# Kernel optimization log

Hardware: AMD Instinct MI355X
Metric: run time of the kernel (lower is better)

## Reference

```python
import jax, jax.numpy as jnp
import numpy as np

N_HEADS = 16

def _rotate_half(x):
    half = x.shape[-1] // 2
    x1, x2 = x[..., :half], x[..., half:]
    return jnp.concatenate([-x2, x1], axis=-1)

def setup_inputs() -> dict:
    key = jax.random.key(0)
    ks = jax.random.split(key, 6)
    B, L, D = 8, 1024, 1280
    hd = D // N_HEADS
    return {
        "hidden_states": jax.random.normal(ks[0], (B, L, D), dtype=jnp.float32),
        "rotary_pos_emb": jax.random.normal(ks[1], (L, hd // 2), dtype=jnp.float32),
        "W_qkv": jax.random.normal(ks[2], (D, 3 * D), dtype=jnp.float32) * 0.02,
        "b_qkv": jax.random.normal(ks[3], (3 * D,), dtype=jnp.float32) * 0.02,
        "W_proj": jax.random.normal(ks[4], (D, D), dtype=jnp.float32) * 0.02,
        "b_proj": jax.random.normal(ks[5], (D,), dtype=jnp.float32) * 0.02,
    }

def reference(hidden_states, rotary_pos_emb, W_qkv, b_qkv, W_proj, b_proj):
    B, L, D = hidden_states.shape
    H = N_HEADS
    hd = D // H
    # QKV projection -> [3, B, H, L, hd]
    qkv = (hidden_states @ W_qkv + b_qkv).reshape(B, L, 3, H, hd)
    qkv = jnp.transpose(qkv, (2, 0, 3, 1, 4))
    q, k, v = qkv[0], qkv[1], qkv[2]
    # rotary embedding: emb = cat([freqs, freqs]) -> [L, hd], broadcast [1,1,L,hd]
    emb = jnp.concatenate([rotary_pos_emb, rotary_pos_emb], axis=-1)
    cos = jnp.cos(emb)[None, None]
    sin = jnp.sin(emb)[None, None]
    q = q * cos + _rotate_half(q) * sin
    k = k * cos + _rotate_half(k) * sin
    # causal SDPA (cu_seqlens is None => is_causal=True)
    scale = 1.0 / jnp.sqrt(jnp.asarray(hd, dtype=q.dtype))
    scores = jnp.einsum("bhqd,bhkd->bhqk", q, k) * scale
    causal = jnp.tril(jnp.ones((L, L), dtype=bool))
    scores = jnp.where(causal, scores, jnp.finfo(scores.dtype).min)
    attn = jax.nn.softmax(scores, axis=-1)
    out = jnp.einsum("bhqk,bhkd->bhqd", attn, v)  # [B,H,L,hd]
    out = jnp.transpose(out, (0, 2, 1, 3)).reshape(B, L, D)
    return out @ W_proj + b_proj
```

## Files before the change

### kernel.cpp

```cpp
#include <hip/hip_runtime.h>
#include <hip/hip_bf16.h>
#include <stdint.h>

#define DEV static __device__ __forceinline__

typedef __attribute__((ext_vector_type(4))) float  f32x4;
typedef __attribute__((ext_vector_type(8))) __bf16 bf16x8;
typedef __attribute__((ext_vector_type(8))) unsigned short u16x8;
typedef __attribute__((ext_vector_type(4))) unsigned short u16x4;
typedef __attribute__((ext_vector_type(4))) float  fvec4;

#define SC2F 0.16129870963914802f

DEV unsigned short f2b(float f) {
  __bf16 h = (__bf16)f;
  unsigned short u; __builtin_memcpy(&u, &h, 2);
  return u;
}
DEV float b2f(unsigned short b) {
  union { unsigned int u; float f; } v; v.u = ((unsigned int)b) << 16;
  return v.f;
}
DEV bf16x8 bzero8() {
  u16x8 z = 0; bf16x8 r; __builtin_memcpy(&r, &z, 16); return r;
}

DEV void gload_lds16(const void* g, void* l) {
  __builtin_amdgcn_global_load_lds(
      (__attribute__((address_space(1))) void*)(uintptr_t)g,
      (__attribute__((address_space(3))) void*)(uintptr_t)l, 16, 0, 0);
}


__global__ void convert_bf16x4(const float* __restrict__ in,
                               unsigned short* __restrict__ out, int n4) {
  int i = blockIdx.x * 256 + threadIdx.x;
  if (i >= n4) return;
  fvec4 v = *(const fvec4*)&in[(size_t)i * 4];
  u16x4 o;
  o[0] = f2b(v[0]); o[1] = f2b(v[1]); o[2] = f2b(v[2]); o[3] = f2b(v[3]);
  *(u16x4*)&out[(size_t)i * 4] = o;
}

__global__ void transpose_f2b(const float* __restrict__ in,
                              unsigned short* __restrict__ out, int R, int C) {
  __shared__ float t[32][33];
  int c0 = blockIdx.x * 32, r0 = blockIdx.y * 32;
  int tx = threadIdx.x & 31, ty = threadIdx.x >> 5;
#pragma unroll
  for (int i = 0; i < 32; i += 8)
    t[ty + i][tx] = in[(size_t)(r0 + ty + i) * C + c0 + tx];
  __syncthreads();
#pragma unroll
  for (int i = 0; i < 32; i += 8)
    out[(size_t)(c0 + ty + i) * R + r0 + tx] = f2b(t[tx][ty + i]);
}

__global__ void rope_table(const float* __restrict__ r, float* __restrict__ c,
                           float* __restrict__ s, int n) {
  int i = blockIdx.x * 256 + threadIdx.x;
  if (i < n) { float v = r[i]; c[i] = cosf(v); s[i] = sinf(v); }
}

template <int EPI>
__global__ __launch_bounds__(512, 2) void gemm256(
    const unsigned short* __restrict__ A, const unsigned short* __restrict__ Bt,
    const float* __restrict__ bias,
    unsigned short* __restrict__ qo, unsigned short* __restrict__ ko,
    unsigned short* __restrict__ vo, float* __restrict__ outf,
    int M, int N, int K) {
  __shared__ __align__(16) unsigned short As[2][256 * 64];
  __shared__ __align__(16) unsigned short Bs[2][256 * 64];
  const int tid = threadIdx.x;
  const int lane = tid & 63, wave = tid >> 6;
  const int wr = wave >> 2, wc = wave & 3;
  const int g = lane >> 4, lr = lane & 15;
  const int nwg = gridDim.x, cpx = nwg >> 3;
  const int swz = (blockIdx.x & 7) * cpx + (blockIdx.x >> 3);
  const int gx = N >> 8;
  const int bx = swz % gx, by = swz / gx;
  const int m0 = by * 256, n0 = bx * 256;
  const int nt = K >> 6;

  f32x4 acc[8][4];
#pragma unroll
  for (int i = 0; i < 8; ++i)
#pragma unroll
    for (int j = 0; j < 4; ++j) acc[i][j] = f32x4{0.f, 0.f, 0.f, 0.f};

#define STAGE256(bi, t)                                                       \
  {                                                                           \
    const int k0s = (t) * 64;                                                 \
    _Pragma("unroll")                                                         \
    for (int it = 0; it < 4; ++it) {                                          \
      int e = (it * 512 + tid) * 8;                                           \
      int r = e >> 6, p = (e >> 3) & 7;                                       \
      int sc = ((p ^ (r & 7)) << 3);                                          \
      gload_lds16(&A[(size_t)(m0 + r) * K + k0s + sc], &As[bi][e]);           \
      gload_lds16(&Bt[(size_t)(n0 + r) * K + k0s + sc], &Bs[bi][e]);          \
    }                                                                         \
  }

  STAGE256(0, 0);
  __syncthreads();

  for (int t = 0; t < nt; ++t) {
    const int cur = t & 1;
    if (t + 1 < nt) STAGE256(cur ^ 1, t + 1);
#pragma unroll
    for (int kk = 0; kk < 2; ++kk) {
      bf16x8 av[8], bv[4];
#pragma unroll
      for (int mf = 0; mf < 8; ++mf) {
        int row = wr * 128 + mf * 16 + lr;
        int ch = (kk * 4 + g) ^ (row & 7);
        av[mf] = *(const bf16x8*)&As[cur][row * 64 + ch * 8];
      }
#pragma unroll
      for (int nf = 0; nf < 4; ++nf) {
        int row = wc * 64 + nf * 16 + lr;
        int ch = (kk * 4 + g) ^ (row & 7);
        bv[nf] = *(const bf16x8*)&Bs[cur][row * 64 + ch * 8];
      }
#pragma unroll
      for (int mf = 0; mf < 8; ++mf)
#pragma unroll
        for (int nf = 0; nf < 4; ++nf)
          acc[mf][nf] = __builtin_amdgcn_mfma_f32_16x16x32_bf16(
              av[mf], bv[nf], acc[mf][nf], 0, 0, 0);
    }
    __syncthreads();
  }
#undef STAGE256

  if (EPI == 0) {
#pragma unroll
    for (int nf = 0; nf < 4; ++nf) {
      int col = n0 + wc * 64 + nf * 16 + lr;
      float bvv = bias[col];
      int s = col / 1280;
      int rem = col - s * 1280;
      int h = rem / 80, d = rem - h * 80;
      unsigned short* dst = (s == 0) ? qo : ((s == 1) ? ko : vo);
#pragma unroll
      for (int mf = 0; mf < 8; ++mf) {
#pragma unroll
        for (int r = 0; r < 4; ++r) {
          int row = m0 + wr * 128 + mf * 16 + g * 4 + r;
          int b = row >> 10, l = row & 1023;
          dst[((size_t)(b * 16 + h) * 1024 + l) * 80 + d] =
              f2b(acc[mf][nf][r] + bvv);
        }
      }
    }
  } else {
#pragma unroll
    for (int mf = 0; mf < 8; ++mf) {
#pragma unroll
      for (int r = 0; r < 4; ++r) {
        int row = m0 + wr * 128 + mf * 16 + g * 4 + r;
#pragma unroll
        for (int nf = 0; nf < 4; ++nf) {
          int col = n0 + wc * 64 + nf * 16 + lr;
          outf[(size_t)row * N + col] = acc[mf][nf][r] + bias[col];
        }
      }
    }
  }
}

template <int EPI>
__global__ __launch_bounds__(256) void gemm128(
    const unsigned short* __restrict__ A, const unsigned short* __restrict__ Bt,
    const float* __restrict__ bias,
    unsigned short* __restrict__ qo, unsigned short* __restrict__ ko,
    unsigned short* __restrict__ vo, float* __restrict__ outf,
    int M, int N, int K) {
  __shared__ __align__(16) unsigned short As[128 * 64];
  __shared__ __align__(16) unsigned short Bs[128 * 64];
  const int tid = threadIdx.x;
  const int lane = tid & 63, wave = tid >> 6;
  const int wr = wave >> 1, wc = wave & 1;
  const int g = lane >> 4, lr = lane & 15;
  const int nwg = gridDim.x, cpx = nwg >> 3;
  const int swz = (blockIdx.x & 7) * cpx + (blockIdx.x >> 3);
  const int gx = N >> 7;
  const int bx = swz % gx, by = swz / gx;
  const int m0 = by * 128, n0 = bx * 128;

  f32x4 acc[4][4];
#pragma unroll
  for (int i = 0; i < 4; ++i)
#pragma unroll
    for (int j = 0; j < 4; ++j) acc[i][j] = f32x4{0.f, 0.f, 0.f, 0.f};

  for (int k0 = 0; k0 < K; k0 += 64) {
#pragma unroll
    for (int it = 0; it < 4; ++it) {
      int e = (it * 256 + tid) * 8;
      int r = e >> 6, p = (e >> 3) & 7;
      int sc = ((p ^ (r & 7)) << 3);
      gload_lds16(&A[(size_t)(m0 + r) * K + k0 + sc], &As[e]);
      gload_lds16(&Bt[(size_t)(n0 + r) * K + k0 + sc], &Bs[e]);
    }
    __syncthreads();
#pragma unroll
    for (int kk = 0; kk < 2; ++kk) {
      bf16x8 av[4], bv[4];
#pragma unroll
      for (int mf = 0; mf < 4; ++mf) {
        int row = wr * 64 + mf * 16 + lr;
        int ch = (kk * 4 + g) ^ (row & 7);
        av[mf] = *(const bf16x8*)&As[row * 64 + ch * 8];
      }
#pragma unroll
      for (int nf = 0; nf < 4; ++nf) {
        int row = wc * 64 + nf * 16 + lr;
        int ch = (kk * 4 + g) ^ (row & 7);
        bv[nf] = *(const bf16x8*)&Bs[row * 64 + ch * 8];
      }
#pragma unroll
      for (int mf = 0; mf < 4; ++mf)
#pragma unroll
        for (int nf = 0; nf < 4; ++nf)
          acc[mf][nf] = __builtin_amdgcn_mfma_f32_16x16x32_bf16(
              av[mf], bv[nf], acc[mf][nf], 0, 0, 0);
    }
    __syncthreads();
  }

  if (EPI == 0) {
#pragma unroll
    for (int nf = 0; nf < 4; ++nf) {
      int col = n0 + wc * 64 + nf * 16 + lr;
      float bvv = bias[col];
      int s = col / 1280;
      int rem = col - s * 1280;
      int h = rem / 80, d = rem - h * 80;
      unsigned short* dst = (s == 0) ? qo : ((s == 1) ? ko : vo);
#pragma unroll
      for (int mf = 0; mf < 4; ++mf) {
#pragma unroll
        for (int r = 0; r < 4; ++r) {
          int row = m0 + wr * 64 + mf * 16 + g * 4 + r;
          int b = row >> 10, l = row & 1023;
          dst[((size_t)(b * 16 + h) * 1024 + l) * 80 + d] =
              f2b(acc[mf][nf][r] + bvv);
        }
      }
    }
  } else {
#pragma unroll
    for (int mf = 0; mf < 4; ++mf) {
#pragma unroll
      for (int r = 0; r < 4; ++r) {
        int row = m0 + wr * 64 + mf * 16 + g * 4 + r;
#pragma unroll
        for (int nf = 0; nf < 4; ++nf) {
          int col = n0 + wc * 64 + nf * 16 + lr;
          outf[(size_t)row * N + col] = acc[mf][nf][r] + bias[col];
        }
      }
    }
  }
}

__global__ void rope_apply(unsigned short* __restrict__ q0,
                           unsigned short* __restrict__ q1,
                           const float* __restrict__ cosT,
                           const float* __restrict__ sinT) {
  int i = blockIdx.x * 256 + threadIdx.x;
  if (i >= 2 * 131072 * 5) return;
  bool isq = (i < 131072 * 5);
  unsigned short* arr = isq ? q0 : q1;
  float sc = isq ? SC2F : 1.0f;
  int rem = isq ? i : (i - 131072 * 5);
  int row = rem / 5, c = rem - (rem / 5) * 5;
  int l = row & 1023;
  size_t base = (size_t)row * 80 + c * 8;
  u16x8 x1 = *(const u16x8*)&arr[base];
  u16x8 x2 = *(const u16x8*)&arr[base + 40];
  const float* cp = &cosT[l * 40 + c * 8];
  const float* sp = &sinT[l * 40 + c * 8];
  u16x8 y1, y2;
#pragma unroll
  for (int j = 0; j < 8; ++j) {
    float a = b2f(x1[j]), b = b2f(x2[j]);
    float cc = cp[j], ss = sp[j];
    y1[j] = f2b((a * cc - b * ss) * sc);
    y2[j] = f2b((b * cc + a * ss) * sc);
  }
  *(u16x8*)&arr[base] = y1;
  *(u16x8*)&arr[base + 40] = y2;
}

__global__ __launch_bounds__(512, 4) void attn_fwd(
    const unsigned short* __restrict__ q, const unsigned short* __restrict__ k,
    const unsigned short* __restrict__ v, unsigned short* __restrict__ o) {
  __shared__ __align__(16) unsigned short Ks[2][5120];
  __shared__ __align__(16) unsigned short Vt[2][5760];
  __shared__ __align__(16) unsigned short Ps[8][2304];

  const int tid = threadIdx.x, lane = tid & 63, wave = tid >> 6;
  const int g = lane >> 4, lr = lane & 15;
  const int bid = blockIdx.x;
  const int t4 = bid >> 7;
  const int qi = (t4 == 0) ? 3 : (t4 == 1) ? 2 : (t4 == 2) ? 0 : 1;
  const int bh = bid & 127;
  const int b = bh >> 4, h = bh & 15;
  const size_t headBase = (size_t)bh * 1024 * 80;
  const int qbase = qi * 256;
  const int wmin = qbase + wave * 32;
  const int nkv = qi * 4 + 4;
  const int vl = tid & 63, vc = tid >> 6;

  bf16x8 qf[2][2], qf2[2];
#pragma unroll
  for (int mf = 0; mf < 2; ++mf) {
    const unsigned short* qr = q + headBase + (size_t)(wmin + mf * 16 + lr) * 80;
    qf[mf][0] = *(const bf16x8*)(qr + g * 8);
    qf[mf][1] = *(const bf16x8*)(qr + 32 + g * 8);
    bf16x8 t = *(const bf16x8*)(qr + 64 + (g & 1) * 8);
    if (g >= 2) t = bzero8();
    qf2[mf] = t;
  }

  float m_r[2] = {-INFINITY, -INFINITY}, l_r[2] = {0.f, 0.f};
  f32x4 o_acc[2][5];
#pragma unroll
  for (int mf = 0; mf < 2; ++mf)
#pragma unroll
    for (int of = 0; of < 5; ++of) o_acc[mf][of] = f32x4{0.f, 0.f, 0.f, 0.f};

  unsigned short* PsW = Ps[wave];

  {
    const unsigned short* vsrc = v + headBase;
    u16x8 p0 = *(const u16x8*)&vsrc[(size_t)vl * 80 + vc * 8];
    u16x8 p1;
    if (tid < 128) p1 = *(const u16x8*)&vsrc[(size_t)vl * 80 + (8 + vc) * 8];
    for (int i = tid; i < 640; i += 512)
      gload_lds16(k + headBase + i * 8, &Ks[0][i * 8]);
#pragma unroll
    for (int j = 0; j < 8; ++j) Vt[0][(vc * 8 + j) * 72 + vl] = p0[j];
    if (tid < 128) {
#pragma unroll
      for (int j = 0; j < 8; ++j) Vt[0][((8 + vc) * 8 + j) * 72 + vl] = p1[j];
    }
  }
  __syncthreads();

  for (int kv = 0; kv < nkv; ++kv) {
    const int bufI = kv & 1, nb = bufI ^ 1;
    const int kvbase = kv * 64;
    const bool doStage = (kv + 1 < nkv);
    const bool active = (kvbase <= wmin + 31);

    u16x8 p0, p1;
    if (doStage) {
      const unsigned short* vsrc = v + headBase + (size_t)(kv + 1) * 5120;
      p0 = *(const u16x8*)&vsrc[(size_t)vl * 80 + vc * 8];
      if (tid < 128) p1 = *(const u16x8*)&vsrc[(size_t)vl * 80 + (8 + vc) * 8];
      const unsigned short* ksrc = k + headBase + (size_t)(kv + 1) * 5120;
      for (int i = tid; i < 640; i += 512)
        gload_lds16(ksrc + i * 8, &Ks[nb][i * 8]);
    }

    if (active) {
      const unsigned short* KsB = Ks[bufI];
      f32x4 s[2][4];
#pragma unroll
      for (int mf = 0; mf < 2; ++mf)
#pragma unroll
        for (int nf = 0; nf < 4; ++nf) s[mf][nf] = f32x4{0.f, 0.f, 0.f, 0.f};
#pragma unroll
      for (int kp = 0; kp < 2; ++kp)
#pragma unroll
        for (int nf = 0; nf < 4; ++nf) {
          bf16x8 kb = *(const bf16x8*)&KsB[(nf * 16 + lr) * 80 + kp * 32 + g * 8];
#pragma unroll
          for (int mf = 0; mf < 2; ++mf)
            s[mf][nf] = __builtin_amdgcn_mfma_f32_16x16x32_bf16(kb, qf[mf][kp],
                                                                s[mf][nf], 0, 0, 0);
        }
#pragma unroll
      for (int nf = 0; nf < 4; ++nf) {
        bf16x8 kb = *(const bf16x8*)&KsB[(nf * 16 + lr) * 80 + 64 + (g & 1) * 8];
#pragma unroll
        for (int mf = 0; mf < 2; ++mf)
          s[mf][nf] = __builtin_amdgcn_mfma_f32_16x16x32_bf16(kb, qf2[mf],
                                                              s[mf][nf], 0, 0, 0);
      }

      const bool maskT = (kvbase + 63 > wmin);
      if (maskT) {
        const int kb0 = kvbase + g * 4;
        const int qq = wmin + lr;
#pragma unroll
        for (int mf = 0; mf < 2; ++mf)
#pragma unroll
          for (int nf = 0; nf < 4; ++nf)
#pragma unroll
            for (int r = 0; r < 4; ++r)
              if (kb0 + nf * 16 + r > qq + mf * 16) s[mf][nf][r] = -INFINITY;
      }
      float mt[2];
#pragma unroll
      for (int mf = 0; mf < 2; ++mf) {
        float a = fmaxf(fmaxf(s[mf][0][0], s[mf][0][1]), fmaxf(s[mf][0][2], s[mf][0][3]));
        float b2 = fmaxf(fmaxf(s[mf][1][0], s[mf][1][1]), fmaxf(s[mf][1][2], s[mf][1][3]));
        float c = fmaxf(fmaxf(s[mf][2][0], s[mf][2][1]), fmaxf(s[mf][2][2], s[mf][2][3]));
        float d = fmaxf(fmaxf(s[mf][3][0], s[mf][3][1]), fmaxf(s[mf][3][2], s[mf][3][3]));
        float m = fmaxf(fmaxf(a, b2), fmaxf(c, d));
        m = fmaxf(m, __shfl_xor(m, 16, 64));
        m = fmaxf(m, __shfl_xor(m, 32, 64));
        mt[mf] = m;
      }
      int ok = (mt[0] <= m_r[0] + 10.0f) && (mt[1] <= m_r[1] + 10.0f);
      const bool need = !__all(ok);
      float fr[2];
      if (need) {
#pragma unroll
        for (int mf = 0; mf < 2; ++mf) {
          float mn = fmaxf(m_r[mf], mt[mf]);
          fr[mf] = exp2f(m_r[mf] - mn);
          m_r[mf] = mn;
        }
      }
      float lt[2] = {0.f, 0.f};
#pragma unroll
      for (int mf = 0; mf < 2; ++mf)
#pragma unroll
        for (int nf = 0; nf < 4; ++nf)
#pragma unroll
          for (int r = 0; r < 4; ++r) {
            float p = exp2f(s[mf][nf][r] - m_r[mf]);
            s[mf][nf][r] = p;
            lt[mf] += p;
          }
#pragma unroll
      for (int mf = 0; mf < 2; ++mf) {
        lt[mf] += __shfl_xor(lt[mf], 16, 64);
        lt[mf] += __shfl_xor(lt[mf], 32, 64);
      }
      if (need) {
#pragma unroll
        for (int mf = 0; mf < 2; ++mf) {
          l_r[mf] = l_r[mf] * fr[mf] + lt[mf];
#pragma unroll
          for (int r = 0; r < 4; ++r) {
            float fro = __shfl(fr[mf], g * 4 + r, 64);
#pragma unroll
            for (int of = 0; of < 5; ++of) o_acc[mf][of][r] *= fro;
          }
        }
      } else {
        l_r[0] += lt[0];
        l_r[1] += lt[1];
      }

#pragma unroll
      for (int mf = 0; mf < 2; ++mf)
#pragma unroll
        for (int nf = 0; nf < 4; ++nf) {
          unsigned w0 = (unsigned)f2b(s[mf][nf][0]) |
                        ((unsigned)f2b(s[mf][nf][1]) << 16);
          unsigned w1 = (unsigned)f2b(s[mf][nf][2]) |
                        ((unsigned)f2b(s[mf][nf][3]) << 16);
          unsigned* dst = (unsigned*)&PsW[(mf * 16 + lr) * 72 + nf * 16 + g * 4];
          dst[0] = w0;
          dst[1] = w1;
        }
    }

    if (doStage) {
#pragma unroll
      for (int j = 0; j < 8; ++j) Vt[nb][(vc * 8 + j) * 72 + vl] = p0[j];
      if (tid < 128) {
#pragma unroll
        for (int j = 0; j < 8; ++j) Vt[nb][((8 + vc) * 8 + j) * 72 + vl] = p1[j];
      }
    }

    if (active) {
      const unsigned short* VtB = Vt[bufI];
#pragma unroll
      for (int kk = 0; kk < 2; ++kk) {
        bf16x8 pa[2];
#pragma unroll
        for (int mf = 0; mf < 2; ++mf)
          pa[mf] = *(const bf16x8*)&PsW[(mf * 16 + lr) * 72 + kk * 32 + g * 8];
#pragma unroll
        for (int of = 0; of < 5; ++of) {
          bf16x8 vv = *(const bf16x8*)&VtB[(of * 16 + lr) * 72 + kk * 32 + g * 8];
#pragma unroll
          for (int mf = 0; mf < 2; ++mf)
            o_acc[mf][of] = __builtin_amdgcn_mfma_f32_16x16x32_bf16(
                pa[mf], vv, o_acc[mf][of], 0, 0, 0);
        }
      }
    }
    __syncthreads();
  }

#pragma unroll
  for (int mf = 0; mf < 2; ++mf) {
    float linv = 1.0f / l_r[mf];
#pragma unroll
    for (int r = 0; r < 4; ++r) {
      float li = __shfl(linv, g * 4 + r, 64);
      int row = wmin + mf * 16 + g * 4 + r;
#pragma unroll
      for (int of = 0; of < 5; ++of)
        o[((size_t)b * 1024 + row) * 1280 + h * 80 + of * 16 + lr] =
            f2b(o_acc[mf][of][r] * li);
    }
  }
}

extern "C" void kernel_launch(void* const* d_in, const int* in_sizes, int n_in,
                              void* d_out, int out_size, void* d_ws, size_t ws_size,
                              hipStream_t stream) {
  const float* X     = (const float*)d_in[0];
  const float* rp    = (const float*)d_in[1];
  const float* Wqkv  = (const float*)d_in[2];
  const float* bqkv  = (const float*)d_in[3];
  const float* Wproj = (const float*)d_in[4];
  const float* bproj = (const float*)d_in[5];
  float* out = (float*)d_out;

  char* ws = (char*)d_ws;
  unsigned short* Xb     = (unsigned short*)(ws);
  unsigned short* Wqkvt  = (unsigned short*)(ws + 20971520);
  unsigned short* Wprojt = (unsigned short*)(ws + 30801920);
  float*          cosT   = (float*)(ws + 34078720);
  float*          sinT   = (float*)(ws + 34242560);
  unsigned short* vb     = (unsigned short*)(ws + 34406400);
  unsigned short* qb     = (unsigned short*)d_out;
  unsigned short* kb     = qb + 10485760;
  unsigned short* Ob     = Xb;

  convert_bf16x4<<<10240, 256, 0, stream>>>(X, Xb, 2621440);
  transpose_f2b<<<dim3(120, 40), 256, 0, stream>>>(Wqkv, Wqkvt, 1280, 3840);
  transpose_f2b<<<dim3(40, 40), 256, 0, stream>>>(Wproj, Wprojt, 1280, 1280);
  rope_table<<<160, 256, 0, stream>>>(rp, cosT, sinT, 40960);
  gemm256<0><<<480, 512, 0, stream>>>(Xb, Wqkvt, bqkv, qb, kb, vb,
                                      nullptr, 8192, 3840, 1280);
  rope_apply<<<5120, 256, 0, stream>>>(qb, kb, cosT, sinT);
  attn_fwd<<<512, 512, 0, stream>>>(qb, kb, vb, Ob);
  gemm128<1><<<640, 256, 0, stream>>>(Ob, Wprojt, bproj, nullptr,
                                      nullptr, nullptr, out, 8192, 1280, 1280);
}
```

Baseline: 349.2 us.

## Write V pre-transposed from QKV GEMM and stage it to LDS asynchronously

The QKV GEMM epilogue now writes V in a per-head [d][l] layout instead of [l][d]. The attention kernel can then copy each V tile straight into LDS with direct global-to-LDS loads, alongside K. This removes the register round-trip and the scalar element-by-element LDS transpose done on every kv step. The trade-off is strided 2-byte stores for V in the GEMM epilogue, which may coalesce poorly. Unused epilogue paths in gemm128 are also removed.

```diff
diff --git a/kernel.cpp b/kernel.cpp
--- a/kernel.cpp
+++ b/kernel.cpp
@@ -141,15 +141,28 @@
       int s = col / 1280;
       int rem = col - s * 1280;
       int h = rem / 80, d = rem - h * 80;
-      unsigned short* dst = (s == 0) ? qo : ((s == 1) ? ko : vo);
-#pragma unroll
-      for (int mf = 0; mf < 8; ++mf) {
-#pragma unroll
-        for (int r = 0; r < 4; ++r) {
-          int row = m0 + wr * 128 + mf * 16 + g * 4 + r;
-          int b = row >> 10, l = row & 1023;
-          dst[((size_t)(b * 16 + h) * 1024 + l) * 80 + d] =
-              f2b(acc[mf][nf][r] + bvv);
+      if (s == 2) {
+#pragma unroll
+        for (int mf = 0; mf < 8; ++mf) {
+#pragma unroll
+          for (int r = 0; r < 4; ++r) {
+            int row = m0 + wr * 128 + mf * 16 + g * 4 + r;
+            int b = row >> 10, l = row & 1023;
+            vo[((size_t)((b * 16 + h) * 80) + d) * 1024 + l] =
+                f2b(acc[mf][nf][r] + bvv);
+          }
+        }
+      } else {
+        unsigned short* dst = (s == 0) ? qo : ko;
+#pragma unroll
+        for (int mf = 0; mf < 8; ++mf) {
+#pragma unroll
+          for (int r = 0; r < 4; ++r) {
+            int row = m0 + wr * 128 + mf * 16 + g * 4 + r;
+            int b = row >> 10, l = row & 1023;
+            dst[((size_t)(b * 16 + h) * 1024 + l) * 80 + d] =
+                f2b(acc[mf][nf][r] + bvv);
+          }
         }
       }
     }
@@ -172,9 +185,7 @@
 template <int EPI>
 __global__ __launch_bounds__(256) void gemm128(
     const unsigned short* __restrict__ A, const unsigned short* __restrict__ Bt,
-    const float* __restrict__ bias,
-    unsigned short* __restrict__ qo, unsigned short* __restrict__ ko,
-    unsigned short* __restrict__ vo, float* __restrict__ outf,
+    const float* __restrict__ bias, float* __restrict__ outf,
     int M, int N, int K) {
   __shared__ __align__(16) unsigned short As[128 * 64];
   __shared__ __align__(16) unsigned short Bs[128 * 64];
@@ -229,37 +240,15 @@
     __syncthreads();
   }
 
-  if (EPI == 0) {
-#pragma unroll
-    for (int nf = 0; nf < 4; ++nf) {
-      int col = n0 + wc * 64 + nf * 16 + lr;
-      float bvv = bias[col];
-      int s = col / 1280;
-      int rem = col - s * 1280;
-      int h = rem / 80, d = rem - h * 80;
-      unsigned short* dst = (s == 0) ? qo : ((s == 1) ? ko : vo);
-#pragma unroll
-      for (int mf = 0; mf < 4; ++mf) {
-#pragma unroll
-        for (int r = 0; r < 4; ++r) {
-          int row = m0 + wr * 64 + mf * 16 + g * 4 + r;
-          int b = row >> 10, l = row & 1023;
-          dst[((size_t)(b * 16 + h) * 1024 + l) * 80 + d] =
-              f2b(acc[mf][nf][r] + bvv);
-        }
-      }
-    }
-  } else {
-#pragma unroll
-    for (int mf = 0; mf < 4; ++mf) {
-#pragma unroll
-      for (int r = 0; r < 4; ++r) {
-        int row = m0 + wr * 64 + mf * 16 + g * 4 + r;
-#pragma unroll
-        for (int nf = 0; nf < 4; ++nf) {
-          int col = n0 + wc * 64 + nf * 16 + lr;
-          outf[(size_t)row * N + col] = acc[mf][nf][r] + bias[col];
-        }
+#pragma unroll
+  for (int mf = 0; mf < 4; ++mf) {
+#pragma unroll
+    for (int r = 0; r < 4; ++r) {
+      int row = m0 + wr * 64 + mf * 16 + g * 4 + r;
+#pragma unroll
+      for (int nf = 0; nf < 4; ++nf) {
+        int col = n0 + wc * 64 + nf * 16 + lr;
+        outf[(size_t)row * N + col] = acc[mf][nf][r] + bias[col];
       }
     }
   }
@@ -296,7 +285,7 @@
 
 __global__ __launch_bounds__(512, 4) void attn_fwd(
     const unsigned short* __restrict__ q, const unsigned short* __restrict__ k,
-    const unsigned short* __restrict__ v, unsigned short* __restrict__ o) {
+    const unsigned short* __restrict__ vt, unsigned short* __restrict__ o) {
   __shared__ __align__(16) unsigned short Ks[2][5120];
   __shared__ __align__(16) unsigned short Vt[2][5760];
   __shared__ __align__(16) unsigned short Ps[8][2304];
@@ -309,10 +298,16 @@
   const int bh = bid & 127;
   const int b = bh >> 4, h = bh & 15;
   const size_t headBase = (size_t)bh * 1024 * 80;
+  const size_t vHeadBase = (size_t)bh * 80 * 1024;
   const int qbase = qi * 256;
   const int wmin = qbase + wave * 32;
   const int nkv = qi * 4 + 4;
-  const int vl = tid & 63, vc = tid >> 6;
+
+  const int vr0 = tid / 9, vcol0 = tid - vr0 * 9;
+  const int vt2 = tid + 512;
+  const int vr1 = vt2 / 9, vcol1 = vt2 - vr1 * 9;
+  const int voff0 = vr0 * 1024 + (vcol0 < 8 ? vcol0 * 8 : 56);
+  const int voff1 = vr1 * 1024 + (vcol1 < 8 ? vcol1 * 8 : 56);
 
   bf16x8 qf[2][2], qf2[2];
 #pragma unroll
@@ -334,39 +329,25 @@
 
   unsigned short* PsW = Ps[wave];
 
-  {
-    const unsigned short* vsrc = v + headBase;
-    u16x8 p0 = *(const u16x8*)&vsrc[(size_t)vl * 80 + vc * 8];
-    u16x8 p1;
-    if (tid < 128) p1 = *(const u16x8*)&vsrc[(size_t)vl * 80 + (8 + vc) * 8];
-    for (int i = tid; i < 640; i += 512)
-      gload_lds16(k + headBase + i * 8, &Ks[0][i * 8]);
-#pragma unroll
-    for (int j = 0; j < 8; ++j) Vt[0][(vc * 8 + j) * 72 + vl] = p0[j];
-    if (tid < 128) {
-#pragma unroll
-      for (int j = 0; j < 8; ++j) Vt[0][((8 + vc) * 8 + j) * 72 + vl] = p1[j];
-    }
-  }
+#define STAGE_KV(kvb, bi)                                                     \
+  {                                                                           \
+    const unsigned short* ksrc = k + headBase + (size_t)(kvb) * 80;           \
+    for (int i = tid; i < 640; i += 512)                                      \
+      gload_lds16(ksrc + i * 8, &Ks[bi][i * 8]);                              \
+    const unsigned short* vsrc = vt + vHeadBase + (kvb);                      \
+    gload_lds16(vsrc + voff0, &Vt[bi][tid * 8]);                              \
+    if (tid < 208) gload_lds16(vsrc + voff1, &Vt[bi][vt2 * 8]);               \
+  }
+
+  STAGE_KV(0, 0);
   __syncthreads();
 
   for (int kv = 0; kv < nkv; ++kv) {
     const int bufI = kv & 1, nb = bufI ^ 1;
     const int kvbase = kv * 64;
-    const bool doStage = (kv + 1 < nkv);
-    const bool active = (kvbase <= wmin + 31);
-
-    u16x8 p0, p1;
-    if (doStage) {
-      const unsigned short* vsrc = v + headBase + (size_t)(kv + 1) * 5120;
-      p0 = *(const u16x8*)&vsrc[(size_t)vl * 80 + vc * 8];
-      if (tid < 128) p1 = *(const u16x8*)&vsrc[(size_t)vl * 80 + (8 + vc) * 8];
-      const unsigned short* ksrc = k + headBase + (size_t)(kv + 1) * 5120;
-      for (int i = tid; i < 640; i += 512)
-        gload_lds16(ksrc + i * 8, &Ks[nb][i * 8]);
-    }
-
-    if (active) {
+    if (kv + 1 < nkv) STAGE_KV((kv + 1) * 64, nb);
+
+    if (kvbase <= wmin + 31) {
       const unsigned short* KsB = Ks[bufI];
       f32x4 s[2][4];
 #pragma unroll
@@ -471,18 +452,7 @@
           dst[0] = w0;
           dst[1] = w1;
         }
-    }
-
-    if (doStage) {
-#pragma unroll
-      for (int j = 0; j < 8; ++j) Vt[nb][(vc * 8 + j) * 72 + vl] = p0[j];
-      if (tid < 128) {
-#pragma unroll
-        for (int j = 0; j < 8; ++j) Vt[nb][((8 + vc) * 8 + j) * 72 + vl] = p1[j];
-      }
-    }
-
-    if (active) {
+
       const unsigned short* VtB = Vt[bufI];
 #pragma unroll
       for (int kk = 0; kk < 2; ++kk) {
@@ -502,6 +472,7 @@
     }
     __syncthreads();
   }
+#undef STAGE_KV
 
 #pragma unroll
   for (int mf = 0; mf < 2; ++mf) {
@@ -548,6 +519,5 @@
                                       nullptr, 8192, 3840, 1280);
   rope_apply<<<5120, 256, 0, stream>>>(qb, kb, cosT, sinT);
   attn_fwd<<<512, 512, 0, stream>>>(qb, kb, vb, Ob);
-  gemm128<1><<<640, 256, 0, stream>>>(Ob, Wprojt, bproj, nullptr,
-                                      nullptr, nullptr, out, 8192, 1280, 1280);
-}
+  gemm128<1><<<640, 256, 0, stream>>>(Ob, Wprojt, bproj, out, 8192, 1280, 1280);
+}
```

After: 329.9 us. 5.5% less time.
